# Kernel optimization log

Hardware: AMD Instinct MI355X
Metric: run time of the kernel (lower is better)

Reference implementation:

```python
import jax, jax.numpy as jnp
import numpy as np

B, S, D, H, NC = 128, 256, 512, 1024, 128

def setup_inputs() -> dict:
    key = jax.random.key(0)
    ks = jax.random.split(key, 12)
    x = jax.random.randint(ks[0], (B, S, 1), 0, NC + 1)
    emb = jax.random.normal(ks[1], (NC + 1, D), dtype=jnp.float32)
    emb = emb.at[0].set(0.0)  # padding_idx=0
    def w(k, shape):
        return jax.random.normal(k, shape, dtype=jnp.float32) * (1.0 / np.sqrt(shape[0]))
    return {
        "x": x, "emb": emb,
        "Wfx": w(ks[2], (D, H)), "Wfh": w(ks[3], (H, H)), "bf": jnp.zeros(H),
        "Wix": w(ks[4], (D, H)), "Wih": w(ks[5], (H, H)), "bi": jnp.zeros(H),
        "Wgx": w(ks[6], (D, H)), "Wgh": w(ks[7], (H, H)), "bg": jnp.zeros(H),
        "Wox": w(ks[8], (D, H)), "Woh": w(ks[9], (H, H)), "bo": jnp.zeros(H),
        "Wph": w(ks[10], (H, NC)), "bp": jnp.zeros(NC),
    }

def reference(x, emb, Wfx, Wfh, bf, Wix, Wih, bi, Wgx, Wgh, bg, Wox, Woh, bo, Wph, bp):
    x_in = x[..., 0].astype(jnp.int32)            # [B,S]
    xe = emb[x_in]                                # [B,S,D]
    # Pre-compute the input-side gate projections for all timesteps (one big GEMM each).
    fx = jnp.einsum('bsd,dh->sbh', xe, Wfx) + bf
    ix = jnp.einsum('bsd,dh->sbh', xe, Wix) + bi
    gx = jnp.einsum('bsd,dh->sbh', xe, Wgx) + bg
    ox = jnp.einsum('bsd,dh->sbh', xe, Wox) + bo
    reset = (x_in > 0).astype(jnp.float32).T      # [S,B]
    def step(carry, inp):
        h, C = carry
        fx_t, ix_t, gx_t, ox_t, r_t = inp
        f = jax.nn.sigmoid(fx_t + h @ Wfh)
        i = jax.nn.sigmoid(ix_t + h @ Wih)
        g = jax.nn.sigmoid(gx_t + h @ Wgh)   # note: sigmoid (as in source), not tanh
        o = jax.nn.sigmoid(ox_t + h @ Woh)
        C = (g * i + C * f) * r_t[:, None]   # zero cell state on padding tokens
        h = o * jnp.tanh(C)
        return (h, C), None
    h0 = jnp.zeros((x.shape[0], Wfh.shape[0]), dtype=jnp.float32)
    (h, _), _ = jax.lax.scan(step, (h0, h0), (fx, ix, gx, ox, reset))
    p = h @ Wph + bp
    return jax.nn.log_softmax(p, axis=1)
```

## Files before the change

kernel.cpp:

```cpp
#include <hip/hip_runtime.h>
#include <hip/hip_bf16.h>

#define BB   128
#define SS   256
#define DD   512
#define HH   1024
#define NCC  128
#define NCLS 129
#define G4   4096
#define NWG  256

typedef __attribute__((ext_vector_type(8)))  short  short8;
typedef __attribute__((ext_vector_type(16))) float  f32x16;

static __device__ __forceinline__ float sigm(float x)  { return 1.0f / (1.0f + __expf(-x)); }
static __device__ __forceinline__ float tanh_(float x) { return 1.0f - 2.0f / (__expf(2.0f * x) + 1.0f); }
static __device__ __forceinline__ unsigned short f2b(float v) {
    __hip_bfloat16 h = __float2bfloat16(v);
    return *reinterpret_cast<unsigned short*>(&h);
}
static __device__ __forceinline__ short8 ld16(const unsigned short* p) {
    return *reinterpret_cast<const short8*>(p);
}

__global__ void k_init(unsigned short* __restrict__ hb0, int* __restrict__ flags) {
    int i = blockIdx.x * 256 + threadIdx.x;
    if (i < BB * HH) hb0[i] = 0;
    if (i < 16384) flags[i] = 0;
}

__global__ void k_conv_wh(const float* __restrict__ Wfh, const float* __restrict__ Wih,
                          const float* __restrict__ Wgh, const float* __restrict__ Woh,
                          unsigned short* __restrict__ WhT) {
    __shared__ float t[32][33];
    int g = blockIdx.z;
    const float* W = (g == 0) ? Wfh : (g == 1) ? Wih : (g == 2) ? Wgh : Woh;
    int h0 = blockIdx.x * 32, k0 = blockIdx.y * 32;
    int tx = threadIdx.x & 31, ty = threadIdx.x >> 5;
    for (int r = 0; r < 4; r++) {
        int k = ty + r * 8;
        t[k][tx] = W[(size_t)(k0 + k) * HH + h0 + tx];
    }
    __syncthreads();
    for (int r = 0; r < 4; r++) {
        int hl = ty + r * 8;
        int j  = (h0 + hl) * 4 + g;
        WhT[(size_t)j * HH + k0 + tx] = f2b(t[tx][hl]);
    }
}

__global__ void k_proj(const float* __restrict__ emb,
                       const float* __restrict__ Wfx, const float* __restrict__ Wix,
                       const float* __restrict__ Wgx, const float* __restrict__ Wox,
                       const float* __restrict__ bf_, const float* __restrict__ bi_,
                       const float* __restrict__ bg_, const float* __restrict__ bo_,
                       float* __restrict__ proj) {
    int c = blockIdx.y;
    int j = blockIdx.x * 256 + threadIdx.x;
    int hcol = j >> 2, g = j & 3;
    const float* Wx = (g == 0) ? Wfx : (g == 1) ? Wix : (g == 2) ? Wgx : Wox;
    const float* bb = (g == 0) ? bf_ : (g == 1) ? bi_ : (g == 2) ? bg_ : bo_;
    float acc = bb[hcol];
    const float* er = emb + (size_t)c * DD;
    for (int d = 0; d < DD; d++) acc += er[d] * Wx[(size_t)d * HH + hcol];
    proj[(size_t)c * G4 + j] = acc;
}

#define LDAB(d, B, L) asm volatile("global_load_dwordx4 %0, %1, off offset:" L " sc0 sc1" \
                                   : "=v"(d) : "v"(B))
#define LD4(A, I) do { \
    LDAB(A[(I)+0], p, "0"); LDAB(A[(I)+1], p, "1024"); \
    LDAB(A[(I)+2], p, "2048"); LDAB(A[(I)+3], p, "3072"); p += 4096; } while (0)
#define LD16(A) do { LD4(A,0); LD4(A,4); LD4(A,8); LD4(A,12); } while (0)

#define WAITA(N, A) asm volatile("s_waitcnt vmcnt(" N ")" : \
    "+v"(A[0]),"+v"(A[1]),"+v"(A[2]),"+v"(A[3]),"+v"(A[4]),"+v"(A[5]),"+v"(A[6]),"+v"(A[7]), \
    "+v"(A[8]),"+v"(A[9]),"+v"(A[10]),"+v"(A[11]),"+v"(A[12]),"+v"(A[13]),"+v"(A[14]),"+v"(A[15]))

#define MF16(A, KB) do { \
    acc0 = __builtin_amdgcn_mfma_f32_32x32x16_bf16(A[0],  breg[(KB)+0],  acc0, 0,0,0); \
    acc1 = __builtin_amdgcn_mfma_f32_32x32x16_bf16(A[1],  breg[(KB)+1],  acc1, 0,0,0); \
    acc0 = __builtin_amdgcn_mfma_f32_32x32x16_bf16(A[2],  breg[(KB)+2],  acc0, 0,0,0); \
    acc1 = __builtin_amdgcn_mfma_f32_32x32x16_bf16(A[3],  breg[(KB)+3],  acc1, 0,0,0); \
    acc0 = __builtin_amdgcn_mfma_f32_32x32x16_bf16(A[4],  breg[(KB)+4],  acc0, 0,0,0); \
    acc1 = __builtin_amdgcn_mfma_f32_32x32x16_bf16(A[5],  breg[(KB)+5],  acc1, 0,0,0); \
    acc0 = __builtin_amdgcn_mfma_f32_32x32x16_bf16(A[6],  breg[(KB)+6],  acc0, 0,0,0); \
    acc1 = __builtin_amdgcn_mfma_f32_32x32x16_bf16(A[7],  breg[(KB)+7],  acc1, 0,0,0); \
    acc0 = __builtin_amdgcn_mfma_f32_32x32x16_bf16(A[8],  breg[(KB)+8],  acc0, 0,0,0); \
    acc1 = __builtin_amdgcn_mfma_f32_32x32x16_bf16(A[9],  breg[(KB)+9],  acc1, 0,0,0); \
    acc0 = __builtin_amdgcn_mfma_f32_32x32x16_bf16(A[10], breg[(KB)+10], acc0, 0,0,0); \
    acc1 = __builtin_amdgcn_mfma_f32_32x32x16_bf16(A[11], breg[(KB)+11], acc1, 0,0,0); \
    acc0 = __builtin_amdgcn_mfma_f32_32x32x16_bf16(A[12], breg[(KB)+12], acc0, 0,0,0); \
    acc1 = __builtin_amdgcn_mfma_f32_32x32x16_bf16(A[13], breg[(KB)+13], acc1, 0,0,0); \
    acc0 = __builtin_amdgcn_mfma_f32_32x32x16_bf16(A[14], breg[(KB)+14], acc0, 0,0,0); \
    acc1 = __builtin_amdgcn_mfma_f32_32x32x16_bf16(A[15], breg[(KB)+15], acc1, 0,0,0); \
} while (0)

#define PRLOAD(DSTA, CLSBUF) do { \
    _Pragma("unroll") \
    for (int r = 0; r < 16; r++) { \
        int row = (r & 3) + 8 * (r >> 2) + 4 * half; \
        const float* pa = proj + (size_t)CLSBUF[row] * G4 + jg; \
        asm volatile("global_load_dword %0, %1, off" : "=v"(DSTA[r]) \
                     : "v"((unsigned long long)pa)); \
    } \
} while (0)

__global__ __launch_bounds__(128, 1)
void k_scan(const int* __restrict__ x, const float* __restrict__ proj,
            const unsigned short* __restrict__ WhT,
            unsigned short* __restrict__ hb0, unsigned short* __restrict__ hb1,
            float* __restrict__ hf32, int* __restrict__ flags) {
    const int wg = blockIdx.x, tid = threadIdx.x;
    const int lane = tid & 63, wv = tid >> 6;
    const int l31 = lane & 31, half = lane >> 5;
    const int mg = wg & 3, ng = wg >> 2;
    const int m0 = mg * 32, n0 = ng * 64;
    const int jg = n0 + wv * 32 + l31;

    short8 breg[64];
    {
        const unsigned short* Bp = WhT + (size_t)jg * HH + half * 8;
        #pragma unroll
        for (int kk = 0; kk < 64; kk++) breg[kk] = ld16(Bp + kk * 16);
    }

    __shared__ float sg[32][68];
    __shared__ int   clsS[2][32];

    float Cst[4] = {0.0f, 0.0f, 0.0f, 0.0f};
    const int urow = tid & 31, uq = tid >> 5;

    if (tid < 32) clsS[0][tid] = x[(size_t)(m0 + tid) * SS];
    __syncthreads();

    const unsigned long long ab0 =
        (unsigned long long)((char*)hb0 + mg * 65536 + lane * 16);
    const unsigned long long ab1 =
        (unsigned long long)((char*)hb1 + mg * 65536 + lane * 16);
    const unsigned long long sb0 = (unsigned long long)((char*)hb0 + mg * 65536
        + ng * 1024 + (urow + ((uq >> 1) << 5)) * 16 + (uq & 1) * 8);
    const unsigned long long sb1 = (unsigned long long)((char*)hb1 + mg * 65536
        + ng * 1024 + (urow + ((uq >> 1) << 5)) * 16 + (uq & 1) * 8);

    const unsigned long long postAddr = (unsigned long long)(flags + (size_t)wg * 32);
    const unsigned long long leafAddr =
        (unsigned long long)(flags + ((size_t)(lane << 2) + mg) * 32);
    const unsigned long long goAddr =
        (unsigned long long)(flags + (size_t)(8192 + mg * 32));
    const bool isAggWave = (ng == 0) && (wv == 0);

    float pr[16];
    PRLOAD(pr, clsS[0]);

    for (int s = 0; s < SS; s++) {
        const int cur = s & 1;
        unsigned long long p = cur ? ab1 : ab0;
        const unsigned long long sb = cur ? sb0 : sb1;

        short8 a0[16], a1[16], a2[16], a3[16];
        LD16(a0);
        LD16(a1);

        f32x16 acc0, acc1;
        #pragma unroll
        for (int r = 0; r < 16; r++) { acc0[r] = 0.0f; acc1[r] = 0.0f; }

        WAITA("16", a0);
        LD16(a2);
        MF16(a0, 0);
        WAITA("16", a1);
        LD16(a3);
        MF16(a1, 16);
        WAITA("16", a2);
        MF16(a2, 32);
        WAITA("0", a3);
        MF16(a3, 48);

        #pragma unroll
        for (int r = 0; r < 16; r++) {
            int row = (r & 3) + 8 * (r >> 2) + 4 * half;
            sg[row][wv * 32 + l31] = sigm(acc0[r] + acc1[r] + pr[r]);
        }
        __syncthreads();

        {
            const float rr = (clsS[cur][urow] > 0) ? 1.0f : 0.0f;
            unsigned short hv[4];
            #pragma unroll
            for (int q = 0; q < 4; q++) {
                float4 gq = *reinterpret_cast<const float4*>(&sg[urow][uq * 16 + q * 4]);
                float cn = (gq.z * gq.y + Cst[q] * gq.x) * rr;
                Cst[q] = cn;
                float hvv = gq.w * tanh_(cn);
                hv[q] = f2b(hvv);
                if (s == SS - 1)
                    hf32[(size_t)(m0 + urow) * HH + ng * 16 + uq * 4 + q] = hvv;
            }
            unsigned long long pk = (unsigned long long)hv[0]
                                  | ((unsigned long long)hv[1] << 16)
                                  | ((unsigned long long)hv[2] << 32)
                                  | ((unsigned long long)hv[3] << 48);
            asm volatile("global_store_dwordx2 %0, %1, off sc0 sc1" :: "v"(sb), "v"(pk) : "memory");
            if (s + 1 < SS && tid < 32)
                clsS[cur ^ 1][tid] = x[(size_t)(m0 + tid) * SS + s + 1];
        }

        if (s < SS - 1) {
            asm volatile("s_waitcnt vmcnt(0)" ::: "memory");
            __syncthreads();
            if (tid == 0) {
                int fv = s + 1;
                asm volatile("global_store_dword %0, %1, off sc0 sc1"
                             :: "v"(postAddr), "v"(fv) : "memory");
            }
            PRLOAD(pr, clsS[cur ^ 1]);
            if (isAggWave) {
                int got;
                do {
                    asm volatile("global_load_dword %0, %1, off sc0 sc1\n\t"
                                 "s_waitcnt vmcnt(0)"
                                 : "=v"(got) : "v"(leafAddr) : "memory");
                } while (__ballot(got >= s + 1) != ~0ull);
                if (tid == 0) {
                    int fv = s + 1;
                    asm volatile("global_store_dword %0, %1, off sc0 sc1"
                                 :: "v"(goAddr), "v"(fv) : "memory");
                }
            } else {
                int got;
                do {
                    asm volatile("global_load_dword %0, %1, off sc0 sc1\n\t"
                                 "s_waitcnt vmcnt(0)"
                                 : "=v"(got) : "v"(goAddr) : "memory");
                } while (got < s + 1);
            }
        }
    }
}

__global__ void k_final(const float* __restrict__ hf32, const float* __restrict__ Wph,
                        const float* __restrict__ bp, float* __restrict__ out) {
    __shared__ float red[128];
    int b = blockIdx.x, c = threadIdx.x;
    const float* hr = hf32 + (size_t)b * HH;
    float acc = bp[c];
    for (int k = 0; k < HH; k++) acc += hr[k] * Wph[(size_t)k * NCC + c];
    red[c] = acc;
    __syncthreads();
    for (int st = 64; st > 0; st >>= 1) {
        if (c < st) red[c] = fmaxf(red[c], red[c + st]);
        __syncthreads();
    }
    float m = red[0];
    __syncthreads();
    red[c] = __expf(acc - m);
    __syncthreads();
    for (int st = 64; st > 0; st >>= 1) {
        if (c < st) red[c] += red[c + st];
        __syncthreads();
    }
    out[(size_t)b * NCC + c] = acc - m - __logf(red[0]);
}

extern "C" void kernel_launch(void* const* d_in, const int* in_sizes, int n_in,
                              void* d_out, int out_size, void* d_ws, size_t ws_size,
                              hipStream_t stream) {
    const int*   x   = (const int*)  d_in[0];
    const float* emb = (const float*)d_in[1];
    const float* Wfx = (const float*)d_in[2];
    const float* Wfh = (const float*)d_in[3];
    const float* bf_ = (const float*)d_in[4];
    const float* Wix = (const float*)d_in[5];
    const float* Wih = (const float*)d_in[6];
    const float* bi_ = (const float*)d_in[7];
    const float* Wgx = (const float*)d_in[8];
    const float* Wgh = (const float*)d_in[9];
    const float* bg_ = (const float*)d_in[10];
    const float* Wox = (const float*)d_in[11];
    const float* Woh = (const float*)d_in[12];
    const float* bo_ = (const float*)d_in[13];
    const float* Wph = (const float*)d_in[14];
    const float* bp_ = (const float*)d_in[15];
    float* out = (float*)d_out;

    char* ws = (char*)d_ws;
    unsigned short* WhT   = (unsigned short*)(ws);
    float*          proj  = (float*)(ws + 8388608);
    int*            flags = (int*)(ws + 10502656);
    unsigned short* hb0   = (unsigned short*)(ws + 10568192);
    unsigned short* hb1   = (unsigned short*)(ws + 10830336);
    float*          hf32  = (float*)(ws + 11092480);

    k_init<<<dim3(512), dim3(256), 0, stream>>>(hb0, flags);
    k_conv_wh<<<dim3(32, 32, 4), dim3(256), 0, stream>>>(Wfh, Wih, Wgh, Woh, WhT);
    k_proj<<<dim3(16, NCLS), dim3(256), 0, stream>>>(emb, Wfx, Wix, Wgx, Wox,
                                                     bf_, bi_, bg_, bo_, proj);
    k_scan<<<dim3(NWG), dim3(128), 0, stream>>>(x, proj, WhT, hb0, hb1, hf32, flags);
    k_final<<<dim3(128), dim3(128), 0, stream>>>(hf32, Wph, bp_, out);
}
```

Baseline: 1.475 ms.

## Split recurrent GEMM over K across waves and reduce partials via LDS

Each of the two waves now covers half of the K dimension (512 of 1024) for both 32-column output tiles, instead of the full K for one tile. This halves the per-wave global loads of the hidden-state A operand each step, since each wave reads only its K half and reuses each A fragment for two MFMAs. The cost is an extra LDS exchange of partial sums and an added __syncthreads per timestep to combine the K halves. The load pipeline is also reshaped into four 8-fragment batches.

```diff
diff --git a/kernel.cpp b/kernel.cpp
--- a/kernel.cpp
+++ b/kernel.cpp
@@ -71,29 +71,22 @@
 #define LD4(A, I) do { \
     LDAB(A[(I)+0], p, "0"); LDAB(A[(I)+1], p, "1024"); \
     LDAB(A[(I)+2], p, "2048"); LDAB(A[(I)+3], p, "3072"); p += 4096; } while (0)
-#define LD16(A) do { LD4(A,0); LD4(A,4); LD4(A,8); LD4(A,12); } while (0)
-
-#define WAITA(N, A) asm volatile("s_waitcnt vmcnt(" N ")" : \
-    "+v"(A[0]),"+v"(A[1]),"+v"(A[2]),"+v"(A[3]),"+v"(A[4]),"+v"(A[5]),"+v"(A[6]),"+v"(A[7]), \
-    "+v"(A[8]),"+v"(A[9]),"+v"(A[10]),"+v"(A[11]),"+v"(A[12]),"+v"(A[13]),"+v"(A[14]),"+v"(A[15]))
-
-#define MF16(A, KB) do { \
-    acc0 = __builtin_amdgcn_mfma_f32_32x32x16_bf16(A[0],  breg[(KB)+0],  acc0, 0,0,0); \
-    acc1 = __builtin_amdgcn_mfma_f32_32x32x16_bf16(A[1],  breg[(KB)+1],  acc1, 0,0,0); \
-    acc0 = __builtin_amdgcn_mfma_f32_32x32x16_bf16(A[2],  breg[(KB)+2],  acc0, 0,0,0); \
-    acc1 = __builtin_amdgcn_mfma_f32_32x32x16_bf16(A[3],  breg[(KB)+3],  acc1, 0,0,0); \
-    acc0 = __builtin_amdgcn_mfma_f32_32x32x16_bf16(A[4],  breg[(KB)+4],  acc0, 0,0,0); \
-    acc1 = __builtin_amdgcn_mfma_f32_32x32x16_bf16(A[5],  breg[(KB)+5],  acc1, 0,0,0); \
-    acc0 = __builtin_amdgcn_mfma_f32_32x32x16_bf16(A[6],  breg[(KB)+6],  acc0, 0,0,0); \
-    acc1 = __builtin_amdgcn_mfma_f32_32x32x16_bf16(A[7],  breg[(KB)+7],  acc1, 0,0,0); \
-    acc0 = __builtin_amdgcn_mfma_f32_32x32x16_bf16(A[8],  breg[(KB)+8],  acc0, 0,0,0); \
-    acc1 = __builtin_amdgcn_mfma_f32_32x32x16_bf16(A[9],  breg[(KB)+9],  acc1, 0,0,0); \
-    acc0 = __builtin_amdgcn_mfma_f32_32x32x16_bf16(A[10], breg[(KB)+10], acc0, 0,0,0); \
-    acc1 = __builtin_amdgcn_mfma_f32_32x32x16_bf16(A[11], breg[(KB)+11], acc1, 0,0,0); \
-    acc0 = __builtin_amdgcn_mfma_f32_32x32x16_bf16(A[12], breg[(KB)+12], acc0, 0,0,0); \
-    acc1 = __builtin_amdgcn_mfma_f32_32x32x16_bf16(A[13], breg[(KB)+13], acc1, 0,0,0); \
-    acc0 = __builtin_amdgcn_mfma_f32_32x32x16_bf16(A[14], breg[(KB)+14], acc0, 0,0,0); \
-    acc1 = __builtin_amdgcn_mfma_f32_32x32x16_bf16(A[15], breg[(KB)+15], acc1, 0,0,0); \
+#define LD8(A) do { LD4(A,0); LD4(A,4); } while (0)
+
+#define WAITB(N, A) asm volatile("s_waitcnt vmcnt(" N ")" : \
+    "+v"(A[0]),"+v"(A[1]),"+v"(A[2]),"+v"(A[3]),"+v"(A[4]),"+v"(A[5]),"+v"(A[6]),"+v"(A[7]))
+
+#define MM(a, b, c) __builtin_amdgcn_mfma_f32_32x32x16_bf16(a, b, c, 0, 0, 0)
+
+#define MF8x2(A, KB) do { \
+    t0e = MM(A[0], breg[((KB)+0)*2+0], t0e); t1e = MM(A[0], breg[((KB)+0)*2+1], t1e); \
+    t0o = MM(A[1], breg[((KB)+1)*2+0], t0o); t1o = MM(A[1], breg[((KB)+1)*2+1], t1o); \
+    t0e = MM(A[2], breg[((KB)+2)*2+0], t0e); t1e = MM(A[2], breg[((KB)+2)*2+1], t1e); \
+    t0o = MM(A[3], breg[((KB)+3)*2+0], t0o); t1o = MM(A[3], breg[((KB)+3)*2+1], t1o); \
+    t0e = MM(A[4], breg[((KB)+4)*2+0], t0e); t1e = MM(A[4], breg[((KB)+4)*2+1], t1e); \
+    t0o = MM(A[5], breg[((KB)+5)*2+0], t0o); t1o = MM(A[5], breg[((KB)+5)*2+1], t1o); \
+    t0e = MM(A[6], breg[((KB)+6)*2+0], t0e); t1e = MM(A[6], breg[((KB)+6)*2+1], t1e); \
+    t0o = MM(A[7], breg[((KB)+7)*2+0], t0o); t1o = MM(A[7], breg[((KB)+7)*2+1], t1o); \
 } while (0)
 
 #define PRLOAD(DSTA, CLSBUF) do { \
@@ -120,12 +113,17 @@
 
     short8 breg[64];
     {
-        const unsigned short* Bp = WhT + (size_t)jg * HH + half * 8;
+        const unsigned short* B0 = WhT + (size_t)(n0 + l31)      * HH + wv * 512 + half * 8;
+        const unsigned short* B1 = WhT + (size_t)(n0 + 32 + l31) * HH + wv * 512 + half * 8;
         #pragma unroll
-        for (int kk = 0; kk < 64; kk++) breg[kk] = ld16(Bp + kk * 16);
+        for (int kk = 0; kk < 32; kk++) {
+            breg[2 * kk + 0] = ld16(B0 + kk * 16);
+            breg[2 * kk + 1] = ld16(B1 + kk * 16);
+        }
     }
 
     __shared__ float sg[32][68];
+    __shared__ float pbuf[2][16][64];
     __shared__ int   clsS[2][32];
 
     float Cst[4] = {0.0f, 0.0f, 0.0f, 0.0f};
@@ -135,9 +133,9 @@
     __syncthreads();
 
     const unsigned long long ab0 =
-        (unsigned long long)((char*)hb0 + mg * 65536 + lane * 16);
+        (unsigned long long)((char*)hb0 + mg * 65536 + wv * 32768 + lane * 16);
     const unsigned long long ab1 =
-        (unsigned long long)((char*)hb1 + mg * 65536 + lane * 16);
+        (unsigned long long)((char*)hb1 + mg * 65536 + wv * 32768 + lane * 16);
     const unsigned long long sb0 = (unsigned long long)((char*)hb0 + mg * 65536
         + ng * 1024 + (urow + ((uq >> 1) << 5)) * 16 + (uq & 1) * 8);
     const unsigned long long sb1 = (unsigned long long)((char*)hb1 + mg * 65536
@@ -158,29 +156,35 @@
         unsigned long long p = cur ? ab1 : ab0;
         const unsigned long long sb = cur ? sb0 : sb1;
 
-        short8 a0[16], a1[16], a2[16], a3[16];
-        LD16(a0);
-        LD16(a1);
-
-        f32x16 acc0, acc1;
+        short8 b0[8], b1[8], b2[8], b3[8];
+        LD8(b0);
+        LD8(b1);
+        LD8(b2);
+
+        f32x16 t0e, t0o, t1e, t1o;
         #pragma unroll
-        for (int r = 0; r < 16; r++) { acc0[r] = 0.0f; acc1[r] = 0.0f; }
-
-        WAITA("16", a0);
-        LD16(a2);
-        MF16(a0, 0);
-        WAITA("16", a1);
-        LD16(a3);
-        MF16(a1, 16);
-        WAITA("16", a2);
-        MF16(a2, 32);
-        WAITA("0", a3);
-        MF16(a3, 48);
+        for (int r = 0; r < 16; r++) { t0e[r] = 0.0f; t0o[r] = 0.0f; t1e[r] = 0.0f; t1o[r] = 0.0f; }
+
+        WAITB("16", b0);
+        MF8x2(b0, 0);
+        LD8(b3);
+        WAITB("16", b1);
+        MF8x2(b1, 8);
+        WAITB("8", b2);
+        MF8x2(b2, 16);
+        WAITB("0", b3);
+        MF8x2(b3, 24);
+
+        #pragma unroll
+        for (int r = 0; r < 16; r++)
+            pbuf[wv][r][lane] = (wv == 0) ? (t1e[r] + t1o[r]) : (t0e[r] + t0o[r]);
+        __syncthreads();
 
         #pragma unroll
         for (int r = 0; r < 16; r++) {
+            float own = (wv == 0) ? (t0e[r] + t0o[r]) : (t1e[r] + t1o[r]);
             int row = (r & 3) + 8 * (r >> 2) + 4 * half;
-            sg[row][wv * 32 + l31] = sigm(acc0[r] + acc1[r] + pr[r]);
+            sg[row][wv * 32 + l31] = sigm(own + pbuf[wv ^ 1][r][lane] + pr[r]);
         }
         __syncthreads();
 
```

Measured after the change: 1.487 ms. Within noise of the previous version (+0.8%).

## Merge prep kernels into one launch and use atomic counter barrier per row group

Applied to the files above, without the earlier changes.

The three setup kernels (init, recurrent weight transpose/convert, input projection table) are merged into one launch dispatched by block index, saving two launch overheads. The per-timestep inter-workgroup barrier in the scan kernel drops the two-level flag tree (leaf flags read by an aggregator wave, then a go flag). Instead each workgroup atomically increments a shared counter for its row group and every workgroup polls that counter until it reaches 64 times the step count. This removes one serial hop of latency per step but concentrates contention on a single atomic and polled address per group. The merged kernel's init blocks zero the flags while the projection blocks run in the same launch, which is safe only because the scan kernel runs afterwards.

```diff
diff --git a/kernel.cpp b/kernel.cpp
--- a/kernel.cpp
+++ b/kernel.cpp
@@ -23,47 +23,54 @@
     return *reinterpret_cast<const short8*>(p);
 }
 
-__global__ void k_init(unsigned short* __restrict__ hb0, int* __restrict__ flags) {
-    int i = blockIdx.x * 256 + threadIdx.x;
-    if (i < BB * HH) hb0[i] = 0;
-    if (i < 16384) flags[i] = 0;
-}
-
-__global__ void k_conv_wh(const float* __restrict__ Wfh, const float* __restrict__ Wih,
-                          const float* __restrict__ Wgh, const float* __restrict__ Woh,
-                          unsigned short* __restrict__ WhT) {
+__global__ void k_pre(unsigned short* __restrict__ hb0, int* __restrict__ flags,
+                      const float* __restrict__ Wfh, const float* __restrict__ Wih,
+                      const float* __restrict__ Wgh, const float* __restrict__ Woh,
+                      unsigned short* __restrict__ WhT,
+                      const float* __restrict__ emb,
+                      const float* __restrict__ Wfx, const float* __restrict__ Wix,
+                      const float* __restrict__ Wgx, const float* __restrict__ Wox,
+                      const float* __restrict__ bf_, const float* __restrict__ bi_,
+                      const float* __restrict__ bg_, const float* __restrict__ bo_,
+                      float* __restrict__ proj) {
     __shared__ float t[32][33];
-    int g = blockIdx.z;
-    const float* W = (g == 0) ? Wfh : (g == 1) ? Wih : (g == 2) ? Wgh : Woh;
-    int h0 = blockIdx.x * 32, k0 = blockIdx.y * 32;
-    int tx = threadIdx.x & 31, ty = threadIdx.x >> 5;
-    for (int r = 0; r < 4; r++) {
-        int k = ty + r * 8;
-        t[k][tx] = W[(size_t)(k0 + k) * HH + h0 + tx];
-    }
-    __syncthreads();
-    for (int r = 0; r < 4; r++) {
-        int hl = ty + r * 8;
-        int j  = (h0 + hl) * 4 + g;
-        WhT[(size_t)j * HH + k0 + tx] = f2b(t[tx][hl]);
-    }
-}
-
-__global__ void k_proj(const float* __restrict__ emb,
-                       const float* __restrict__ Wfx, const float* __restrict__ Wix,
-                       const float* __restrict__ Wgx, const float* __restrict__ Wox,
-                       const float* __restrict__ bf_, const float* __restrict__ bi_,
-                       const float* __restrict__ bg_, const float* __restrict__ bo_,
-                       float* __restrict__ proj) {
-    int c = blockIdx.y;
-    int j = blockIdx.x * 256 + threadIdx.x;
-    int hcol = j >> 2, g = j & 3;
-    const float* Wx = (g == 0) ? Wfx : (g == 1) ? Wix : (g == 2) ? Wgx : Wox;
-    const float* bb = (g == 0) ? bf_ : (g == 1) ? bi_ : (g == 2) ? bg_ : bo_;
-    float acc = bb[hcol];
-    const float* er = emb + (size_t)c * DD;
-    for (int d = 0; d < DD; d++) acc += er[d] * Wx[(size_t)d * HH + hcol];
-    proj[(size_t)c * G4 + j] = acc;
+    const int bid = blockIdx.x;
+    if (bid < 512) {
+        int i = bid * 256 + threadIdx.x;
+        if (i < BB * HH) hb0[i] = 0;
+        if (i < 16384) flags[i] = 0;
+        return;
+    }
+    if (bid < 4608) {
+        int b = bid - 512;
+        int bx = b & 31, by = (b >> 5) & 31, g = b >> 10;
+        const float* W = (g == 0) ? Wfh : (g == 1) ? Wih : (g == 2) ? Wgh : Woh;
+        int h0 = bx * 32, k0 = by * 32;
+        int tx = threadIdx.x & 31, ty = threadIdx.x >> 5;
+        for (int r = 0; r < 4; r++) {
+            int k = ty + r * 8;
+            t[k][tx] = W[(size_t)(k0 + k) * HH + h0 + tx];
+        }
+        __syncthreads();
+        for (int r = 0; r < 4; r++) {
+            int hl = ty + r * 8;
+            int j  = (h0 + hl) * 4 + g;
+            WhT[(size_t)j * HH + k0 + tx] = f2b(t[tx][hl]);
+        }
+        return;
+    }
+    {
+        int b = bid - 4608;
+        int c = b >> 4;
+        int j = (b & 15) * 256 + threadIdx.x;
+        int hcol = j >> 2, g = j & 3;
+        const float* Wx = (g == 0) ? Wfx : (g == 1) ? Wix : (g == 2) ? Wgx : Wox;
+        const float* bb = (g == 0) ? bf_ : (g == 1) ? bi_ : (g == 2) ? bg_ : bo_;
+        float acc = bb[hcol];
+        const float* er = emb + (size_t)c * DD;
+        for (int d = 0; d < DD; d++) acc += er[d] * Wx[(size_t)d * HH + hcol];
+        proj[(size_t)c * G4 + j] = acc;
+    }
 }
 
 #define LDAB(d, B, L) asm volatile("global_load_dwordx4 %0, %1, off offset:" L " sc0 sc1" \
@@ -143,12 +150,8 @@
     const unsigned long long sb1 = (unsigned long long)((char*)hb1 + mg * 65536
         + ng * 1024 + (urow + ((uq >> 1) << 5)) * 16 + (uq & 1) * 8);
 
-    const unsigned long long postAddr = (unsigned long long)(flags + (size_t)wg * 32);
-    const unsigned long long leafAddr =
-        (unsigned long long)(flags + ((size_t)(lane << 2) + mg) * 32);
-    const unsigned long long goAddr =
+    const unsigned long long ctrAddr =
         (unsigned long long)(flags + (size_t)(8192 + mg * 32));
-    const bool isAggWave = (ng == 0) && (wv == 0);
 
     float pr[16];
     PRLOAD(pr, clsS[0]);
@@ -210,31 +213,18 @@
             asm volatile("s_waitcnt vmcnt(0)" ::: "memory");
             __syncthreads();
             if (tid == 0) {
-                int fv = s + 1;
-                asm volatile("global_store_dword %0, %1, off sc0 sc1"
-                             :: "v"(postAddr), "v"(fv) : "memory");
+                int one = 1;
+                asm volatile("global_atomic_add %0, %1, off"
+                             :: "v"(ctrAddr), "v"(one) : "memory");
             }
             PRLOAD(pr, clsS[cur ^ 1]);
-            if (isAggWave) {
-                int got;
-                do {
-                    asm volatile("global_load_dword %0, %1, off sc0 sc1\n\t"
-                                 "s_waitcnt vmcnt(0)"
-                                 : "=v"(got) : "v"(leafAddr) : "memory");
-                } while (__ballot(got >= s + 1) != ~0ull);
-                if (tid == 0) {
-                    int fv = s + 1;
-                    asm volatile("global_store_dword %0, %1, off sc0 sc1"
-                                 :: "v"(goAddr), "v"(fv) : "memory");
-                }
-            } else {
-                int got;
-                do {
-                    asm volatile("global_load_dword %0, %1, off sc0 sc1\n\t"
-                                 "s_waitcnt vmcnt(0)"
-                                 : "=v"(got) : "v"(goAddr) : "memory");
-                } while (got < s + 1);
-            }
+            const int tv = (s + 1) << 6;
+            int got;
+            do {
+                asm volatile("global_load_dword %0, %1, off sc0 sc1\n\t"
+                             "s_waitcnt vmcnt(0)"
+                             : "=v"(got) : "v"(ctrAddr) : "memory");
+            } while (got < tv);
         }
     }
 }
@@ -292,10 +282,9 @@
     unsigned short* hb1   = (unsigned short*)(ws + 10830336);
     float*          hf32  = (float*)(ws + 11092480);
 
-    k_init<<<dim3(512), dim3(256), 0, stream>>>(hb0, flags);
-    k_conv_wh<<<dim3(32, 32, 4), dim3(256), 0, stream>>>(Wfh, Wih, Wgh, Woh, WhT);
-    k_proj<<<dim3(16, NCLS), dim3(256), 0, stream>>>(emb, Wfx, Wix, Wgx, Wox,
-                                                     bf_, bi_, bg_, bo_, proj);
+    k_pre<<<dim3(6672), dim3(256), 0, stream>>>(hb0, flags, Wfh, Wih, Wgh, Woh, WhT,
+                                                emb, Wfx, Wix, Wgx, Wox,
+                                                bf_, bi_, bg_, bo_, proj);
     k_scan<<<dim3(NWG), dim3(128), 0, stream>>>(x, proj, WhT, hb0, hb1, hf32, flags);
     k_final<<<dim3(128), dim3(128), 0, stream>>>(hf32, Wph, bp_, out);
 }
```

New measurement: 1.416 ms. 4.1% less time.
